# Kernel optimization log

Measured on AMD Instinct MI355X. Metric: run time of the kernel, lower is better.

## Reference

```python
import jax, jax.numpy as jnp
import numpy as np

PI = float(np.pi)


def _conv2d(x, w, b, pad):
    out = jax.lax.conv_general_dilated(x, w, (1, 1), ((pad, pad), (pad, pad)),
                                       dimension_numbers=('NCHW', 'OIHW', 'NCHW'))
    return out + b[None, :, None, None]


def _group_norm(x, gamma, beta, groups, eps=1e-5):
    B, C, h, w = x.shape
    xg = x.reshape(B, groups, C // groups, h, w)
    mu = xg.mean(axis=(2, 3, 4), keepdims=True)
    var = xg.var(axis=(2, 3, 4), keepdims=True)
    xn = ((xg - mu) / jnp.sqrt(var + eps)).reshape(B, C, h, w)
    return xn * gamma[None, :, None, None] + beta[None, :, None, None]


def _l2n(x, eps=1e-12):
    return x / jnp.maximum(jnp.linalg.norm(x, axis=1, keepdims=True), eps)


def _dense_sift(x):
    # kornia DenseSIFTDescriptor defaults: 8 ang bins, 4x4 spatial bins,
    # spatial_bin_size=4, rootsift=True, clipval=0.2, stride=1, padding=1
    eps = 1e-10
    NA = 8
    # 'diff' spatial gradient with replicate padding, normalized (/2)
    xp = jnp.pad(x, ((0, 0), (0, 0), (1, 1), (1, 1)), mode='edge')
    gx = (xp[:, :, 1:-1, 2:] - xp[:, :, 1:-1, :-2]) * 0.5
    gy = (xp[:, :, 2:, 1:-1] - xp[:, :, :-2, 1:-1]) * 0.5
    mag = jnp.sqrt(gx * gx + gy * gy + eps)[:, 0]           # [B,H,W]
    ori = jnp.arctan2(gy, gx + eps)[:, 0] + 2.0 * PI
    o_big = NA * ori / (2.0 * PI)
    bo0f = jnp.floor(o_big)
    wo1_ = o_big - bo0f
    wo0 = (1.0 - wo1_) * mag
    wo1 = wo1_ * mag
    bo0 = bo0f.astype(jnp.int32) % NA
    bo1 = (bo0 + 1) % NA
    bins = jnp.arange(NA).reshape(1, NA, 1, 1)
    ang = ((bo0[:, None] == bins).astype(x.dtype) * wo0[:, None]
           + (bo1[:, None] == bins).astype(x.dtype) * wo1[:, None])  # [B,8,H,W]
    # SIFT pooling kernel ksize=4 (triangle weights), conv pad=2 -> H+1,W+1
    xc2 = np.array([0.5, 1.5, 1.5, 0.5], np.float32)
    pool1 = np.outer(xc2, xc2) / 4.0
    pk = jnp.asarray(np.tile(pool1[None, None], (NA, 1, 1, 1)))  # depthwise [8,1,4,4]
    pooled = jax.lax.conv_general_dilated(ang, pk, (1, 1), ((2, 2), (2, 2)),
                dimension_numbers=('NCHW', 'OIHW', 'NCHW'), feature_group_count=NA)
    # identity reshape conv: 128 = 8 ang * 4*4 spatial bins, pad=1 -> back to H,W
    rk = jnp.asarray(np.eye(128, dtype=np.float32).reshape(128, NA, 4, 4))
    out = jax.lax.conv_general_dilated(pooled, rk, (1, 1), ((1, 1), (1, 1)),
                dimension_numbers=('NCHW', 'OIHW', 'NCHW'))
    out = jnp.clip(_l2n(out), 0.0, 0.2)
    out = _l2n(out)
    l1 = jnp.maximum(jnp.sum(jnp.abs(out), axis=1, keepdims=True), 1e-12)
    return jnp.sqrt(out / l1 + eps)  # rootsift


def _joint_bilateral(x, guide, ksize=5, sigma_color=0.1, sigma_space=1.5):
    pad = ksize // 2
    ax = np.arange(ksize, dtype=np.float32) - ksize // 2
    g1 = np.exp(-ax ** 2 / (2.0 * sigma_space ** 2))
    g1 = g1 / g1.sum()
    sk = np.outer(g1, g1)  # normalized 5x5 gaussian space kernel
    xp = jnp.pad(x, ((0, 0), (0, 0), (pad, pad), (pad, pad)), mode='reflect')
    gp = jnp.pad(guide, ((0, 0), (0, 0), (pad, pad), (pad, pad)), mode='reflect')
    h, w = x.shape[2], x.shape[3]
    inv = -0.5 / (sigma_color ** 2)
    num = jnp.zeros_like(x)
    den = jnp.zeros((x.shape[0], 1, h, w), x.dtype)
    for dy in range(ksize):           # fixed 5x5 tap loop, accumulated in-place
        for dx in range(ksize):
            gs = gp[:, :, dy:dy + h, dx:dx + w]
            cd = jnp.sum(jnp.abs(gs - guide), axis=1, keepdims=True) ** 2  # l1 squared
            wgt = sk[dy, dx] * jnp.exp(inv * cd)
            num = num + wgt * xp[:, :, dy:dy + h, dx:dx + w]
            den = den + wgt
    return num / den


def _forward(x, gt, w1, b1, g1w, g1b, w2, b2, g2w, g2b, w3, b3, g3w, g3b,
             w4, b4, g4w, g4b, w5, b5):
    orig = x
    f = _dense_sift(x)
    f = jax.nn.relu(_group_norm(_conv2d(f, w1, b1, 2), g1w, g1b, 8))
    f = jax.nn.relu(_group_norm(_conv2d(f, w2, b2, 1), g2w, g2b, 8))
    f = jax.nn.relu(_group_norm(_conv2d(f, w3, b3, 1), g3w, g3b, 4))
    f = jax.nn.relu(_group_norm(_conv2d(f, w4, b4, 1), g4w, g4b, 4))
    f = _conv2d(f, w5, b5, 1)
    # rgb_to_yuv(gt)[:, 1:] as guidance
    r, g, b = gt[:, 0], gt[:, 1], gt[:, 2]
    u = -0.147 * r - 0.289 * g + 0.436 * b
    v = 0.615 * r - 0.515 * g - 0.100 * b
    guide = jnp.stack([u, v], axis=1)
    f = _joint_bilateral(f, guide)

    def _rescale(c, lo, hi):
        c = (c - c.min()) / (c.max() - c.min() + 1e-6)  # global min/max over B,H,W
        c = jnp.clip(c, 0.0, 1.0)
        return c * (hi - lo) + lo

    U = _rescale(f[:, 0], -0.436, 0.436)
    V = _rescale(f[:, 1], -0.615, 0.615)
    Y = orig[:, 0]
    R = Y + 1.14 * V
    G = Y - 0.396 * U - 0.581 * V
    B = Y + 2.029 * U
    return jnp.stack([R, G, B], axis=1)


def setup_inputs() -> dict:
    key = jax.random.key(0)
    ks = jax.random.split(key, 16)
    B = 4
    d = {
        'x': jax.random.uniform(ks[0], (B, 1, 270, 512), jnp.float32),
        'gt': jax.random.uniform(ks[1], (B, 3, 270, 512), jnp.float32),
        'w1': jax.random.normal(ks[2], (64, 128, 5, 5), jnp.float32) * 0.02,
        'b1': jnp.zeros((64,), jnp.float32),
        'g1w': jnp.ones((64,), jnp.float32), 'g1b': jnp.zeros((64,), jnp.float32),
        'w2': jax.random.normal(ks[3], (32, 64, 3, 3), jnp.float32) * 0.04,
        'b2': jnp.zeros((32,), jnp.float32),
        'g2w': jnp.ones((32,), jnp.float32), 'g2b': jnp.zeros((32,), jnp.float32),
        'w3': jax.random.normal(ks[4], (16, 32, 3, 3), jnp.float32) * 0.05,
        'b3': jnp.zeros((16,), jnp.float32),
        'g3w': jnp.ones((16,), jnp.float32), 'g3b': jnp.zeros((16,), jnp.float32),
        'w4': jax.random.normal(ks[5], (8, 16, 3, 3), jnp.float32) * 0.08,
        'b4': jnp.zeros((8,), jnp.float32),
        'g4w': jnp.ones((8,), jnp.float32), 'g4b': jnp.zeros((8,), jnp.float32),
        'w5': jax.random.normal(ks[6], (2, 8, 3, 3), jnp.float32) * 0.1,
        'b5': jnp.zeros((2,), jnp.float32),
    }
    return d


def reference(x, gt, w1, b1, g1w, g1b, w2, b2, g2w, g2b, w3, b3, g3w, g3b,
              w4, b4, g4w, g4b, w5, b5):
    return _forward(x, gt, w1, b1, g1w, g1b, w2, b2, g2w, g2b, w3, b3, g3w, g3b,
                    w4, b4, g4w, g4b, w5, b5)
```

## Files before the change

kernel.cpp:

```cpp
#include <hip/hip_runtime.h>

constexpr int NB  = 4;
constexpr int IH  = 270;
constexpr int IW  = 512;
constexpr int NPIX = IH * IW;
constexpr int PH  = 271;
constexpr int PW  = 513;
constexpr float TWO_PI_F = 6.28318530717958647692f;

typedef short  bf16x8 __attribute__((ext_vector_type(8)));
typedef float floatx4 __attribute__((ext_vector_type(4)));

__device__ inline short f2bf(float x) {
  union { float f; unsigned u; } un; un.f = x;
  unsigned r = un.u + 0x7fff + ((un.u >> 16) & 1);
  return (short)(r >> 16);
}

__global__ __launch_bounds__(256) void pooled_kernel(
    const float* __restrict__ x, float* __restrict__ pooled) {
  const int b = blockIdx.z;
  const int px0 = blockIdx.x * 16, py0 = blockIdx.y * 16;
  __shared__ float wo0s[19][19];
  __shared__ float wo1s[19][19];
  __shared__ int   bo0s[19][19];
  const float* xb = x + (size_t)b * NPIX;

  for (int t = threadIdx.x; t < 19 * 19; t += 256) {
    int r = t / 19, c = t % 19;
    int gy = py0 - 2 + r, gx = px0 - 2 + c;
    float w0 = 0.f, w1v = 0.f; int b0 = 0;
    if (gy >= 0 && gy < IH && gx >= 0 && gx < IW) {
      int xm = gx > 0 ? gx - 1 : 0, xp = gx < IW - 1 ? gx + 1 : IW - 1;
      int ym = gy > 0 ? gy - 1 : 0, yp = gy < IH - 1 ? gy + 1 : IH - 1;
      float gxv = (xb[gy * IW + xp] - xb[gy * IW + xm]) * 0.5f;
      float gyv = (xb[yp * IW + gx] - xb[ym * IW + gx]) * 0.5f;
      float mag = sqrtf(gxv * gxv + gyv * gyv + 1e-10f);
      float ori = atan2f(gyv, gxv + 1e-10f) + TWO_PI_F;
      float obig = ori * (8.0f / TWO_PI_F);
      float bf = floorf(obig);
      float w1_ = obig - bf;
      w0  = (1.0f - w1_) * mag;
      w1v = w1_ * mag;
      b0  = ((int)bf) & 7;
    }
    wo0s[r][c] = w0; wo1s[r][c] = w1v; bo0s[r][c] = b0;
  }
  __syncthreads();

  const int t = threadIdx.x;
  const int lx = t % 16, ly = t / 16;
  const int py = py0 + ly, px = px0 + lx;
  if (py >= PH || px >= PW) return;

  const float pwt[4] = {0.25f, 0.75f, 0.75f, 0.25f};
  float acc[8] = {0, 0, 0, 0, 0, 0, 0, 0};
  for (int i = 0; i < 4; i++) {
    for (int j = 0; j < 4; j++) {
      int r = ly + i, c = lx + j;
      float w0 = wo0s[r][c], w1v = wo1s[r][c];
      int b0 = bo0s[r][c];
      int b1i = (b0 + 1) & 7;
      float pw = pwt[i] * pwt[j];
      #pragma unroll
      for (int a = 0; a < 8; a++) {
        float add = (a == b0 ? w0 : 0.f) + (a == b1i ? w1v : 0.f);
        acc[a] = fmaf(pw, add, acc[a]);
      }
    }
  }
  float* pb = pooled + (size_t)b * 8 * PH * PW;
  #pragma unroll
  for (int a = 0; a < 8; a++) pb[((size_t)a * PH + py) * PW + px] = acc[a];
}

__global__ __launch_bounds__(256) void sift_scalars_kernel(
    const float* __restrict__ pooled, float* __restrict__ s1g) {
  const int b = blockIdx.z;
  const int x0 = blockIdx.x * 16, y0 = blockIdx.y * 16;
  __shared__ float pt[8][19][19];
  const float* pb = pooled + (size_t)b * 8 * PH * PW;
  for (int t = threadIdx.x; t < 8 * 19 * 19; t += 256) {
    int a = t / 361, rc = t % 361, r = rc / 19, c = rc % 19;
    int gy = y0 - 1 + r, gx = x0 - 1 + c;
    float v = 0.f;
    if (gy >= 0 && gy < PH && gx >= 0 && gx < PW) v = pb[((size_t)a * PH + gy) * PW + gx];
    pt[a][r][c] = v;
  }
  __syncthreads();
  const int t = threadIdx.x;
  const int lx = t % 16, ly = t / 16;
  const int y = y0 + ly, x = x0 + lx;
  if (y >= IH) return;

  float sum2 = 0.f;
  for (int c = 0; c < 128; c++) {
    int a = c >> 4, i = (c >> 2) & 3, j = c & 3;
    float p = pt[a][ly + i][lx + j];
    sum2 = fmaf(p, p, sum2);
  }
  float s1 = 1.0f / fmaxf(sqrtf(sum2), 1e-12f);
  float st2 = 0.f, st = 0.f;
  for (int c = 0; c < 128; c++) {
    int a = c >> 4, i = (c >> 2) & 3, j = c & 3;
    float p = pt[a][ly + i][lx + j];
    float tv = fminf(p * s1, 0.2f);
    st2 = fmaf(tv, tv, st2);
    st += tv;
  }
  float s2 = 1.0f / fmaxf(sqrtf(st2), 1e-12f);
  float l1 = fmaxf(s2 * st, 1e-12f);
  float g = s2 / l1;
  float* o = s1g + (size_t)b * 2 * NPIX;
  o[y * IW + x] = s1;
  o[NPIX + y * IW + x] = g;
}

__global__ void repack_kernel(const float* __restrict__ w, float* __restrict__ wT,
                              int CO, int CI, int KK) {
  int i = blockIdx.x * 256 + threadIdx.x;
  int total = CO * CI * KK;
  if (i >= total) return;
  int o = i / (CI * KK);
  int r = i % (CI * KK);
  int ci = r / KK, kk = r % KK;
  wT[(kk * CI + ci) * CO + o] = w[i];
}

__global__ void mfma_pack_kernel(const float* __restrict__ w, short* __restrict__ wB,
                                 int CO, int CI, int KK) {
  int CHUNKS = (CI + 31) / 32;
  int GG = (CO + 15) / 16;
  int total = GG * CHUNKS * KK * 512;
  for (int i = blockIdx.x * 256 + threadIdx.x; i < total; i += gridDim.x * 256) {
    int j = i & 7, l = (i >> 3) & 63, f = i >> 9;
    int t = f % KK; int fc = f / KK; int cc = fc % CHUNKS; int g = fc / CHUNKS;
    int ci = cc * 32 + ((l >> 4) << 3) + j;
    int co = g * 16 + (l & 15);
    float v = (ci < CI && co < CO) ? w[((size_t)co * CI + ci) * KK + t] : 0.f;
    wB[i] = f2bf(v);
  }
}

__global__ __launch_bounds__(256) void conv1_mfma_kernel(
    const float* __restrict__ pooled, const float* __restrict__ s1g,
    const short* __restrict__ w1B, const float* __restrict__ bias,
    float* __restrict__ out, float* __restrict__ stats) {
  const int b = blockIdx.z;
  const int x0 = blockIdx.x * 16, y0 = blockIdx.y * 16;
  __shared__ __align__(16) char smem_raw[52128];
  short* desc = (short*)smem_raw;
  float* pt   = (float*)(smem_raw + 32000);
  float* sc   = (float*)(smem_raw + 48928);
  float* cout = (float*)smem_raw;

  const int tid = threadIdx.x;
  const int wave = tid >> 6, lane = tid & 63;
  const int quad = lane >> 4, lm = lane & 15;
  const int mh = wave & 1, pp = wave >> 1;

  const float* pb = pooled + (size_t)b * 8 * PH * PW;
  for (int t = tid; t < 8 * 23 * 23; t += 256) {
    int a = t / 529, rc = t % 529, r = rc / 23, c = rc % 23;
    int gy = y0 - 3 + r, gx = x0 - 3 + c;
    float v = 0.f;
    if (gy >= 0 && gy < PH && gx >= 0 && gx < PW) v = pb[((size_t)a * PH + gy) * PW + gx];
    pt[t] = v;
  }
  const float* sb = s1g + (size_t)b * 2 * NPIX;
  for (int t = tid; t < 400; t += 256) {
    int r = t / 20, c = t % 20;
    int gy = y0 - 2 + r, gx = x0 - 2 + c;
    float a0 = 0.f, a1 = 0.f;
    if (gy >= 0 && gy < IH && gx >= 0 && gx < IW) {
      a0 = sb[gy * IW + gx];
      a1 = sb[NPIX + gy * IW + gx];
    }
    sc[t] = a0; sc[400 + t] = a1;
  }

  const int laneoff = lm * 40 + quad * 8;
  floatx4 acc[2][8];
  #pragma unroll
  for (int n = 0; n < 2; n++)
    #pragma unroll
    for (int m = 0; m < 8; m++) acc[n][m] = (floatx4){0.f, 0.f, 0.f, 0.f};

  for (int cc = 0; cc < 4; cc++) {
    __syncthreads();
    for (int v = tid; v < 3200; v += 256) {
      int pos = v % 400, cg = v / 400;
      int r = pos / 20, c = pos % 20;
      int gy = y0 - 2 + r, gx = x0 - 2 + c;
      bool ok = (gy >= 0 && gy < IH && gx >= 0 && gx < IW);
      int ci0 = cc * 32 + cg * 4;
      int a = ci0 >> 4, i = (ci0 >> 2) & 3;
      float s1v = sc[pos], gv = sc[400 + pos];
      const float* prow = pt + a * 529 + (r + i) * 23 + c;
      unsigned short o4[4];
      #pragma unroll
      for (int q = 0; q < 4; q++) {
        float p = prow[q];
        float val = ok ? sqrtf(fminf(p * s1v, 0.2f) * gv + 1e-10f) : 0.f;
        o4[q] = (unsigned short)f2bf(val);
      }
      uint2 pk;
      pk.x = (unsigned)o4[0] | ((unsigned)o4[1] << 16);
      pk.y = (unsigned)o4[2] | ((unsigned)o4[3] << 16);
      *(uint2*)(desc + pos * 40 + cg * 4) = pk;
    }
    __syncthreads();

    #pragma unroll
    for (int ky = 0; ky < 5; ky++) {
      #pragma unroll
      for (int kx = 0; kx < 5; kx++) {
        bf16x8 bfr[2];
        #pragma unroll
        for (int ng = 0; ng < 2; ng++) {
          int f = ((pp * 2 + ng) * 4 + cc) * 25 + ky * 5 + kx;
          bfr[ng] = *(const bf16x8*)(w1B + ((size_t)f << 9) + (lane << 3));
        }
        bf16x8 av[8];
        #pragma unroll
        for (int m = 0; m < 8; m++) {
          int mt = mh * 8 + m;
          av[m] = *(const bf16x8*)(desc + (mt + ky) * 800 + kx * 40 + laneoff);
        }
        #pragma unroll
        for (int ng = 0; ng < 2; ng++)
          #pragma unroll
          for (int m = 0; m < 8; m++)
            acc[ng][m] = __builtin_amdgcn_mfma_f32_16x16x32_bf16(av[m], bfr[ng], acc[ng][m], 0, 0, 0);
      }
    }
  }

  float* ob = out + (size_t)b * 64 * NPIX;
  for (int h = 0; h < 2; h++) {
    __syncthreads();
    if (pp == h) {
      #pragma unroll
      for (int ng = 0; ng < 2; ng++)
        #pragma unroll
        for (int m = 0; m < 8; m++)
          #pragma unroll
          for (int r = 0; r < 4; r++)
            cout[(ng * 16 + lm) * 261 + (mh * 8 + m) * 16 + quad * 4 + r] = acc[ng][m][r];
    }
    __syncthreads();
    for (int v = tid; v < 8192; v += 256) {
      int col = v >> 8, px = v & 255;
      int y = y0 + (px >> 4), x = x0 + (px & 15);
      if (y < IH)
        ob[(size_t)(h * 32 + col) * NPIX + y * IW + x] = cout[col * 261 + px] + bias[h * 32 + col];
    }
    int col = tid >> 3, seg = tid & 7;
    int co = h * 32 + col;
    float bv = bias[co];
    float sum = 0.f, sq = 0.f;
    #pragma unroll
    for (int rr = 0; rr < 2; rr++) {
      int row = seg * 2 + rr;
      if (y0 + row < IH) {
        #pragma unroll
        for (int k = 0; k < 16; k++) {
          float vv = cout[col * 261 + row * 16 + k] + bv;
          sum += vv; sq += vv * vv;
        }
      }
    }
    sum += __shfl_down(sum, 4); sq += __shfl_down(sq, 4);
    sum += __shfl_down(sum, 2); sq += __shfl_down(sq, 2);
    sum += __shfl_down(sum, 1); sq += __shfl_down(sq, 1);
    if ((tid & 7) == 0) {
      atomicAdd(&stats[(b * 64 + co) * 2], sum);
      atomicAdd(&stats[(b * 64 + co) * 2 + 1], sq);
    }
  }
}

template <int CI, int CO, bool STATS>
__global__ __launch_bounds__(256) void convk3_mfma_kernel(
    const float* __restrict__ xin, const short* __restrict__ wB,
    const float* __restrict__ bias, const float* __restrict__ cA,
    const float* __restrict__ cB, float* __restrict__ stats,
    float* __restrict__ out) {
  constexpr int CHUNKS = CI / 32;
  constexpr int G = CO / 16;
  constexpr int WPG = 4 / G;
  constexpr int TPW = G;
  constexpr int CIS = CHUNKS * 32 + 8;
  const int b = blockIdx.z;
  const int x0 = blockIdx.x * 8, y0 = blockIdx.y * 8;
  __shared__ __align__(16) short tile[100 * CIS];
  __shared__ float cout[CO * 65];
  const int tid = threadIdx.x;
  const int wave = tid >> 6, lane = tid & 63;
  const int quad = lane >> 4, lm = lane & 15;
  const int g = wave / WPG, mh = wave % WPG;

  const float* xb = xin + (size_t)b * CI * NPIX;
  const float* cAb = cA + b * CI;
  const float* cBb = cB + b * CI;
  for (int v = tid; v < (CI / 2) * 100; v += 256) {
    int cp = v / 100, pos = v % 100;
    int r = pos / 10, c = pos % 10;
    int gy = y0 - 1 + r, gx = x0 - 1 + c;
    float v0 = 0.f, v1 = 0.f;
    if (gy >= 0 && gy < IH && gx >= 0 && gx < IW) {
      v0 = fmaxf(fmaf(xb[(size_t)(2 * cp) * NPIX + gy * IW + gx], cAb[2 * cp], cBb[2 * cp]), 0.f);
      v1 = fmaxf(fmaf(xb[(size_t)(2 * cp + 1) * NPIX + gy * IW + gx], cAb[2 * cp + 1], cBb[2 * cp + 1]), 0.f);
    }
    unsigned pk = (unsigned)(unsigned short)f2bf(v0) |
                  ((unsigned)(unsigned short)f2bf(v1) << 16);
    *(unsigned*)(tile + pos * CIS + 2 * cp) = pk;
  }
  __syncthreads();

  int abase[TPW];
  #pragma unroll
  for (int i = 0; i < TPW; i++) {
    int pixel = (mh * TPW + i) * 16 + lm;
    abase[i] = ((pixel >> 3) * 10 + (pixel & 7)) * CIS + quad * 8;
  }

  floatx4 acc[TPW];
  #pragma unroll
  for (int i = 0; i < TPW; i++) acc[i] = (floatx4){0.f, 0.f, 0.f, 0.f};

  #pragma unroll
  for (int cc = 0; cc < CHUNKS; cc++) {
    #pragma unroll
    for (int ky = 0; ky < 3; ky++) {
      bf16x8 bfr[3];
      #pragma unroll
      for (int kx = 0; kx < 3; kx++) {
        int f = (g * CHUNKS + cc) * 9 + ky * 3 + kx;
        bfr[kx] = *(const bf16x8*)(wB + ((size_t)f << 9) + (lane << 3));
      }
      #pragma unroll
      for (int kx = 0; kx < 3; kx++) {
        #pragma unroll
        for (int i = 0; i < TPW; i++) {
          bf16x8 av = *(const bf16x8*)(tile + abase[i] + cc * 32 + (ky * 10 + kx) * CIS);
          acc[i] = __builtin_amdgcn_mfma_f32_16x16x32_bf16(av, bfr[kx], acc[i], 0, 0, 0);
        }
      }
    }
  }
  #pragma unroll
  for (int i = 0; i < TPW; i++) {
    #pragma unroll
    for (int r = 0; r < 4; r++) {
      int pixel = (mh * TPW + i) * 16 + quad * 4 + r;
      cout[(g * 16 + lm) * 65 + pixel] = acc[i][r];
    }
  }
  __syncthreads();
  float* ob = out + (size_t)b * CO * NPIX;
  for (int v = tid; v < CO * 64; v += 256) {
    int co = v >> 6, pix = v & 63;
    int y = y0 + (pix >> 3), x = x0 + (pix & 7);
    if (y < IH) ob[(size_t)co * NPIX + y * IW + x] = cout[co * 65 + pix] + bias[co];
  }
  if (STATS) {
    constexpr int TPC = 256 / CO;
    constexpr int PXT = 64 / TPC;
    int col = tid / TPC, seg = tid % TPC;
    float bv = bias[col];
    float sum = 0.f, sq = 0.f;
    for (int k = 0; k < PXT; k++) {
      int p = seg * PXT + k;
      if (y0 + (p >> 3) < IH) {
        float vv = cout[col * 65 + p] + bv;
        sum += vv; sq += vv * vv;
      }
    }
    #pragma unroll
    for (int off = TPC / 2; off > 0; off >>= 1) {
      sum += __shfl_down(sum, off);
      sq  += __shfl_down(sq, off);
    }
    if (seg == 0) {
      atomicAdd(&stats[(b * CO + col) * 2], sum);
      atomicAdd(&stats[(b * CO + col) * 2 + 1], sq);
    }
  }
}

template <int CI, int CO, int OPT, bool STATS>
__global__ __launch_bounds__(256) void convs_kernel(
    const float* __restrict__ xin, const float* __restrict__ wT,
    const float* __restrict__ bias, const float* __restrict__ cA,
    const float* __restrict__ cB, float* __restrict__ stats,
    float* __restrict__ out) {
  const int b = blockIdx.z;
  const int x0 = blockIdx.x * 8, y0 = blockIdx.y * 8;
  __shared__ float tile[CI][10][10];
  __shared__ float ssum[CO], ssq[CO];
  if (STATS && threadIdx.x < CO) { ssum[threadIdx.x] = 0.f; ssq[threadIdx.x] = 0.f; }
  const float* xb = xin + (size_t)b * CI * NPIX;
  const float* cAb = cA + b * CI;
  const float* cBb = cB + b * CI;
  for (int t = threadIdx.x; t < CI * 100; t += 256) {
    int ci = t / 100, rc = t % 100, r = rc / 10, c = rc % 10;
    int gy = y0 - 1 + r, gx = x0 - 1 + c;
    float v = 0.f;
    if (gy >= 0 && gy < IH && gx >= 0 && gx < IW)
      v = fmaxf(fmaf(xb[(size_t)ci * NPIX + gy * IW + gx], cAb[ci], cBb[ci]), 0.f);
    tile[ci][r][c] = v;
  }
  __syncthreads();
  const int t = threadIdx.x;
  const int px = t % 64, og = t / 64;
  const int pyy = px / 8, pxx = px % 8;
  const int oc0 = og * OPT;
  const int y = y0 + pyy, x = x0 + pxx;
  if (og < CO / OPT) {
    float acc[OPT] = {};
    for (int ky = 0; ky < 3; ky++) {
      for (int kx = 0; kx < 3; kx++) {
        const float* wrow = wT + (size_t)((ky * 3 + kx) * CI) * CO + oc0;
        for (int ci = 0; ci < CI; ci++) {
          float v = tile[ci][pyy + ky][pxx + kx];
          #pragma unroll
          for (int o = 0; o < OPT; o++) acc[o] = fmaf(v, wrow[ci * CO + o], acc[o]);
        }
      }
    }
    if (y < IH) {
      float* ob = out + (size_t)b * CO * NPIX;
      #pragma unroll
      for (int o = 0; o < OPT; o++) {
        float vv = acc[o] + bias[oc0 + o];
        ob[(size_t)(oc0 + o) * NPIX + y * IW + x] = vv;
        if (STATS) {
          atomicAdd(&ssum[oc0 + o], vv);
          atomicAdd(&ssq[oc0 + o], vv * vv);
        }
      }
    }
  }
  if (STATS) {
    __syncthreads();
    if (threadIdx.x < CO) {
      atomicAdd(&stats[(b * CO + threadIdx.x) * 2], ssum[threadIdx.x]);
      atomicAdd(&stats[(b * CO + threadIdx.x) * 2 + 1], ssq[threadIdx.x]);
    }
  }
}

__global__ void gn_coef_kernel(const float* __restrict__ stats,
                               const float* __restrict__ gamma,
                               const float* __restrict__ beta,
                               float* __restrict__ cA, float* __restrict__ cB,
                               int C, int chper) {
  int i = blockIdx.x * 64 + threadIdx.x;
  if (i >= NB * C) return;
  int b = i / C, c = i % C;
  int g0 = (c / chper) * chper;
  double S = 0.0, S2 = 0.0;
  for (int k = 0; k < chper; k++) {
    S  += (double)stats[(b * C + g0 + k) * 2];
    S2 += (double)stats[(b * C + g0 + k) * 2 + 1];
  }
  double Nd = (double)chper * NPIX;
  double mu = S / Nd;
  double var = S2 / Nd - mu * mu;
  double rstd = 1.0 / sqrt(var + 1e-5);
  float A = (float)rstd * gamma[c];
  cA[i] = A;
  cB[i] = beta[c] - (float)mu * A;
}

__global__ __launch_bounds__(256) void bilateral_kernel(
    const float* __restrict__ f, const float* __restrict__ gt,
    float* __restrict__ out) {
  const int b = blockIdx.z;
  const int x0 = blockIdx.x * 16, y0 = blockIdx.y * 16;
  __shared__ float gu[20][20], gv[20][20], f0s[20][20], f1s[20][20];
  const float* gtb = gt + (size_t)b * 3 * NPIX;
  const float* fb = f + (size_t)b * 2 * NPIX;
  for (int t = threadIdx.x; t < 400; t += 256) {
    int r = t / 20, c = t % 20;
    int gy = y0 - 2 + r, gx = x0 - 2 + c;
    if (gy < 0) gy = -gy;
    if (gy > IH - 1) gy = 2 * (IH - 1) - gy;
    if (gx < 0) gx = -gx;
    if (gx > IW - 1) gx = 2 * (IW - 1) - gx;
    int p = gy * IW + gx;
    float rr = gtb[p], gg = gtb[NPIX + p], bb = gtb[2 * NPIX + p];
    gu[r][c]  = -0.147f * rr - 0.289f * gg + 0.436f * bb;
    gv[r][c]  =  0.615f * rr - 0.515f * gg - 0.100f * bb;
    f0s[r][c] = fb[p];
    f1s[r][c] = fb[NPIX + p];
  }
  __syncthreads();
  const int t = threadIdx.x;
  const int lx = t % 16, ly = t / 16;
  const int y = y0 + ly, x = x0 + lx;
  if (y >= IH) return;

  float g1v[5];
  {
    float s = 0.f;
    #pragma unroll
    for (int k = 0; k < 5; k++) {
      float a = (float)(k - 2);
      g1v[k] = expf(-a * a / 4.5f);
      s += g1v[k];
    }
    #pragma unroll
    for (int k = 0; k < 5; k++) g1v[k] /= s;
  }
  float cu = gu[ly + 2][lx + 2], cv = gv[ly + 2][lx + 2];
  float num0 = 0.f, num1 = 0.f, den = 0.f;
  #pragma unroll
  for (int dy = 0; dy < 5; dy++) {
    #pragma unroll
    for (int dx = 0; dx < 5; dx++) {
      float du = fabsf(gu[ly + dy][lx + dx] - cu) + fabsf(gv[ly + dy][lx + dx] - cv);
      float wgt = g1v[dy] * g1v[dx] * expf(-50.0f * du * du);
      num0 = fmaf(wgt, f0s[ly + dy][lx + dx], num0);
      num1 = fmaf(wgt, f1s[ly + dy][lx + dx], num1);
      den += wgt;
    }
  }
  float* ob = out + (size_t)b * 2 * NPIX;
  ob[y * IW + x] = num0 / den;
  ob[NPIX + y * IW + x] = num1 / den;
}

__global__ __launch_bounds__(256) void minmax_partial_kernel(
    const float* __restrict__ bil, float* __restrict__ part) {
  float mn0 = 1e30f, mx0 = -1e30f, mn1 = 1e30f, mx1 = -1e30f;
  for (size_t i = (size_t)blockIdx.x * 256 + threadIdx.x; i < (size_t)NB * NPIX;
       i += 256 * 256) {
    int b = (int)(i / NPIX), p = (int)(i % NPIX);
    float v0 = bil[(size_t)b * 2 * NPIX + p];
    float v1 = bil[(size_t)b * 2 * NPIX + NPIX + p];
    mn0 = fminf(mn0, v0); mx0 = fmaxf(mx0, v0);
    mn1 = fminf(mn1, v1); mx1 = fmaxf(mx1, v1);
  }
  __shared__ float sh[4][256];
  sh[0][threadIdx.x] = mn0; sh[1][threadIdx.x] = mx0;
  sh[2][threadIdx.x] = mn1; sh[3][threadIdx.x] = mx1;
  __syncthreads();
  for (int off = 128; off > 0; off >>= 1) {
    if (threadIdx.x < off) {
      sh[0][threadIdx.x] = fminf(sh[0][threadIdx.x], sh[0][threadIdx.x + off]);
      sh[1][threadIdx.x] = fmaxf(sh[1][threadIdx.x], sh[1][threadIdx.x + off]);
      sh[2][threadIdx.x] = fminf(sh[2][threadIdx.x], sh[2][threadIdx.x + off]);
      sh[3][threadIdx.x] = fmaxf(sh[3][threadIdx.x], sh[3][threadIdx.x + off]);
    }
    __syncthreads();
  }
  if (threadIdx.x == 0) {
    part[blockIdx.x * 4 + 0] = sh[0][0];
    part[blockIdx.x * 4 + 1] = sh[1][0];
    part[blockIdx.x * 4 + 2] = sh[2][0];
    part[blockIdx.x * 4 + 3] = sh[3][0];
  }
}

__global__ __launch_bounds__(256) void minmax_final_kernel(
    const float* __restrict__ part, float* __restrict__ mm) {
  __shared__ float sh[4][256];
  int t = threadIdx.x;
  sh[0][t] = part[t * 4 + 0];
  sh[1][t] = part[t * 4 + 1];
  sh[2][t] = part[t * 4 + 2];
  sh[3][t] = part[t * 4 + 3];
  __syncthreads();
  for (int off = 128; off > 0; off >>= 1) {
    if (t < off) {
      sh[0][t] = fminf(sh[0][t], sh[0][t + off]);
      sh[1][t] = fmaxf(sh[1][t], sh[1][t + off]);
      sh[2][t] = fminf(sh[2][t], sh[2][t + off]);
      sh[3][t] = fmaxf(sh[3][t], sh[3][t + off]);
    }
    __syncthreads();
  }
  if (t == 0) {
    mm[0] = sh[0][0]; mm[1] = sh[1][0]; mm[2] = sh[2][0]; mm[3] = sh[3][0];
  }
}

__global__ __launch_bounds__(256) void final_kernel(
    const float* __restrict__ bil, const float* __restrict__ x,
    const float* __restrict__ mm, float* __restrict__ out) {
  int i = blockIdx.x * 256 + threadIdx.x;
  if (i >= NB * NPIX) return;
  int b = i / NPIX, p = i % NPIX;
  float f0 = bil[(size_t)b * 2 * NPIX + p];
  float f1 = bil[(size_t)b * 2 * NPIX + NPIX + p];
  float U = (f0 - mm[0]) / (mm[1] - mm[0] + 1e-6f);
  U = fminf(fmaxf(U, 0.f), 1.f) * 0.872f - 0.436f;
  float V = (f1 - mm[2]) / (mm[3] - mm[2] + 1e-6f);
  V = fminf(fmaxf(V, 0.f), 1.f) * 1.23f - 0.615f;
  float Y = x[(size_t)b * NPIX + p];
  float* ob = out + (size_t)b * 3 * NPIX;
  ob[p]            = Y + 1.14f * V;
  ob[NPIX + p]     = Y - 0.396f * U - 0.581f * V;
  ob[2 * NPIX + p] = Y + 2.029f * U;
}

extern "C" void kernel_launch(void* const* d_in, const int* in_sizes, int n_in,
                              void* d_out, int out_size, void* d_ws, size_t ws_size,
                              hipStream_t stream) {
  const float* x   = (const float*)d_in[0];
  const float* gt  = (const float*)d_in[1];
  const float* w1  = (const float*)d_in[2];
  const float* b1  = (const float*)d_in[3];
  const float* g1w = (const float*)d_in[4];
  const float* g1b = (const float*)d_in[5];
  const float* w2  = (const float*)d_in[6];
  const float* b2  = (const float*)d_in[7];
  const float* g2w = (const float*)d_in[8];
  const float* g2b = (const float*)d_in[9];
  const float* w3  = (const float*)d_in[10];
  const float* b3  = (const float*)d_in[11];
  const float* g3w = (const float*)d_in[12];
  const float* g3b = (const float*)d_in[13];
  const float* w4  = (const float*)d_in[14];
  const float* b4  = (const float*)d_in[15];
  const float* g4w = (const float*)d_in[16];
  const float* g4b = (const float*)d_in[17];
  const float* w5  = (const float*)d_in[18];
  const float* b5  = (const float*)d_in[19];
  float* out = (float*)d_out;

  char* ws = (char*)d_ws;
  float* statsF = (float*)ws;
  float* stats1 = statsF;
  float* stats2 = statsF + 512;
  float* stats3 = statsF + 768;
  float* stats4 = statsF + 896;
  float* c1A = (float*)(ws + 4096);
  float* c1B = c1A + 256;
  float* c2A = c1B + 256;
  float* c2B = c2A + 128;
  float* c3A = c2B + 128;
  float* c3B = c3A + 64;
  float* c4A = c3B + 64;
  float* c4B = c4A + 32;
  float* mmpart = (float*)(ws + 8192);
  float* mm     = (float*)(ws + 12288);
  float* fbase  = (float*)(ws + 16384);
  size_t off = 0;
  float* pooled = fbase + off; off += 4452864;
  float* s1g    = fbase + off; off += 1105920;
  short* w1B    = (short*)(fbase + off); off += 102400;
  short* w2B    = (short*)(fbase + off); off += 9216;
  short* w3B    = (short*)(fbase + off); off += 2304;
  float* w4T    = fbase + off; off += 1152;
  float* w5T    = fbase + off; off += 256;
  float* bufA   = fbase + off; off += 35389440;
  float* bufB   = fbase + off; off += 17694720;
  float* c5     = pooled;
  float* bilat  = pooled + 1105920;

  hipMemsetAsync(statsF, 0, 960 * sizeof(float), stream);

  mfma_pack_kernel<<<800, 256, 0, stream>>>(w1, w1B, 64, 128, 25);
  mfma_pack_kernel<<<72, 256, 0, stream>>>(w2, w2B, 32, 64, 9);
  mfma_pack_kernel<<<18, 256, 0, stream>>>(w3, w3B, 16, 32, 9);
  repack_kernel<<<(8 * 16 * 9 + 255) / 256, 256, 0, stream>>>(w4, w4T, 8, 16, 9);
  repack_kernel<<<(2 * 8 * 9 + 255) / 256, 256, 0, stream>>>(w5, w5T, 2, 8, 9);

  pooled_kernel<<<dim3(33, 17, NB), 256, 0, stream>>>(x, pooled);
  sift_scalars_kernel<<<dim3(32, 17, NB), 256, 0, stream>>>(pooled, s1g);
  conv1_mfma_kernel<<<dim3(32, 17, NB), 256, 0, stream>>>(pooled, s1g, w1B, b1, bufA, stats1);
  gn_coef_kernel<<<(NB * 64 + 63) / 64, 64, 0, stream>>>(stats1, g1w, g1b, c1A, c1B, 64, 8);

  convk3_mfma_kernel<64, 32, true><<<dim3(64, 34, NB), 256, 0, stream>>>(
      bufA, w2B, b2, c1A, c1B, stats2, bufB);
  gn_coef_kernel<<<(NB * 32 + 63) / 64, 64, 0, stream>>>(stats2, g2w, g2b, c2A, c2B, 32, 4);

  convk3_mfma_kernel<32, 16, true><<<dim3(64, 34, NB), 256, 0, stream>>>(
      bufB, w3B, b3, c2A, c2B, stats3, bufA);
  gn_coef_kernel<<<(NB * 16 + 63) / 64, 64, 0, stream>>>(stats3, g3w, g3b, c3A, c3B, 16, 4);

  convs_kernel<16, 8, 2, true><<<dim3(64, 34, NB), 256, 0, stream>>>(
      bufA, w4T, b4, c3A, c3B, stats4, bufB);
  gn_coef_kernel<<<(NB * 8 + 63) / 64, 64, 0, stream>>>(stats4, g4w, g4b, c4A, c4B, 8, 2);

  convs_kernel<8, 2, 1, false><<<dim3(64, 34, NB), 256, 0, stream>>>(
      bufB, w5T, b5, c4A, c4B, nullptr, c5);

  bilateral_kernel<<<dim3(32, 17, NB), 256, 0, stream>>>(c5, gt, bilat);
  minmax_partial_kernel<<<256, 256, 0, stream>>>(bilat, mmpart);
  minmax_final_kernel<<<1, 256, 0, stream>>>(mmpart, mm);
  final_kernel<<<(NB * NPIX + 255) / 256, 256, 0, stream>>>(bilat, x, mm, out);

  (void)in_sizes; (void)n_in; (void)out_size; (void)ws_size;
}
```

Baseline: 1.555 ms.

## Fuse GN coefficients, weight packing and min/max into neighbouring kernels; retile convs

Merges the five weight-repack launches into one prep kernel and computes the GroupNorm coefficients inside each consumer conv kernel, which removes the separate gn_coef launches. The min/max reduction now happens in the bilateral kernel through wave shuffles and ordered-key atomics, replacing two reduction kernels. Conv1 stages pooled planes per channel chunk to cut shared memory, adds an occupancy hint and re-splits the MFMA tiles across waves. The 3x3 convs move to 16x8 output tiles to get more reuse per block. The cost is redundant coefficient math in every block, extra atomics, and a different register/LDS balance.

```diff
diff --git a/kernel.cpp b/kernel.cpp
--- a/kernel.cpp
+++ b/kernel.cpp
@@ -15,6 +15,74 @@
   union { float f; unsigned u; } un; un.f = x;
   unsigned r = un.u + 0x7fff + ((un.u >> 16) & 1);
   return (short)(r >> 16);
+}
+__device__ inline unsigned fkey(float f) {
+  unsigned u = __float_as_uint(f);
+  return (u & 0x80000000u) ? ~u : (u | 0x80000000u);
+}
+__device__ inline float funkey(unsigned k) {
+  unsigned u = (k & 0x80000000u) ? (k ^ 0x80000000u) : ~k;
+  return __uint_as_float(u);
+}
+__device__ inline void gn_coef_thread(const float* __restrict__ stats,
+                                      const float* __restrict__ gamma,
+                                      const float* __restrict__ beta,
+                                      float* cA, float* cB, int C, int chper, int b) {
+  int c = threadIdx.x;
+  if (c < C) {
+    int g0 = (c / chper) * chper;
+    float S = 0.f, S2 = 0.f;
+    for (int k = 0; k < chper; k++) {
+      S  += stats[(b * C + g0 + k) * 2];
+      S2 += stats[(b * C + g0 + k) * 2 + 1];
+    }
+    double Nd = (double)chper * NPIX;
+    double mu = (double)S / Nd;
+    double var = (double)S2 / Nd - mu * mu;
+    double rstd = 1.0 / sqrt(var + 1e-5);
+    float A = (float)rstd * gamma[c];
+    cA[c] = A;
+    cB[c] = beta[c] - (float)mu * A;
+  }
+}
+
+__device__ inline void mfma_pack_one(const float* __restrict__ w, short* __restrict__ wB,
+                                     int i, int CO, int CI, int KK, int CHUNKS) {
+  int j = i & 7, l = (i >> 3) & 63, f = i >> 9;
+  int t = f % KK; int fc = f / KK; int cc = fc % CHUNKS; int g = fc / CHUNKS;
+  int ci = cc * 32 + ((l >> 4) << 3) + j;
+  int co = g * 16 + (l & 15);
+  float v = (ci < CI && co < CO) ? w[((size_t)co * CI + ci) * KK + t] : 0.f;
+  wB[i] = f2bf(v);
+}
+__device__ inline void repack_one(const float* __restrict__ w, float* __restrict__ wT,
+                                  int i, int CO, int CI, int KK) {
+  int o = i / (CI * KK);
+  int r = i % (CI * KK);
+  int ci = r / KK, kk = r % KK;
+  wT[(kk * CI + ci) * CO + o] = w[i];
+}
+__global__ __launch_bounds__(256) void prep_kernel(
+    const float* __restrict__ w1, const float* __restrict__ w2,
+    const float* __restrict__ w3, const float* __restrict__ w4,
+    const float* __restrict__ w5,
+    short* __restrict__ w1B, short* __restrict__ w2B, short* __restrict__ w3B,
+    float* __restrict__ w4T, float* __restrict__ w5T) {
+  constexpr int N1 = 4 * 4 * 25 * 512;
+  constexpr int N2 = 2 * 2 * 9 * 512;
+  constexpr int N3 = 1 * 1 * 9 * 512;
+  constexpr int N4 = 8 * 16 * 9;
+  constexpr int N5 = 2 * 8 * 9;
+  int i = blockIdx.x * 256 + threadIdx.x;
+  if (i < N1) { mfma_pack_one(w1, w1B, i, 64, 128, 25, 4); return; }
+  i -= N1;
+  if (i < N2) { mfma_pack_one(w2, w2B, i, 32, 64, 9, 2); return; }
+  i -= N2;
+  if (i < N3) { mfma_pack_one(w3, w3B, i, 16, 32, 9, 1); return; }
+  i -= N3;
+  if (i < N4) { repack_one(w4, w4T, i, 8, 16, 9); return; }
+  i -= N4;
+  if (i < N5) { repack_one(w5, w5T, i, 2, 8, 9); return; }
 }
 
 __global__ __launch_bounds__(256) void pooled_kernel(
@@ -116,57 +184,23 @@
   o[NPIX + y * IW + x] = g;
 }
 
-__global__ void repack_kernel(const float* __restrict__ w, float* __restrict__ wT,
-                              int CO, int CI, int KK) {
-  int i = blockIdx.x * 256 + threadIdx.x;
-  int total = CO * CI * KK;
-  if (i >= total) return;
-  int o = i / (CI * KK);
-  int r = i % (CI * KK);
-  int ci = r / KK, kk = r % KK;
-  wT[(kk * CI + ci) * CO + o] = w[i];
-}
-
-__global__ void mfma_pack_kernel(const float* __restrict__ w, short* __restrict__ wB,
-                                 int CO, int CI, int KK) {
-  int CHUNKS = (CI + 31) / 32;
-  int GG = (CO + 15) / 16;
-  int total = GG * CHUNKS * KK * 512;
-  for (int i = blockIdx.x * 256 + threadIdx.x; i < total; i += gridDim.x * 256) {
-    int j = i & 7, l = (i >> 3) & 63, f = i >> 9;
-    int t = f % KK; int fc = f / KK; int cc = fc % CHUNKS; int g = fc / CHUNKS;
-    int ci = cc * 32 + ((l >> 4) << 3) + j;
-    int co = g * 16 + (l & 15);
-    float v = (ci < CI && co < CO) ? w[((size_t)co * CI + ci) * KK + t] : 0.f;
-    wB[i] = f2bf(v);
-  }
-}
-
-__global__ __launch_bounds__(256) void conv1_mfma_kernel(
+__global__ __launch_bounds__(256, 4) void conv1_mfma_kernel(
     const float* __restrict__ pooled, const float* __restrict__ s1g,
     const short* __restrict__ w1B, const float* __restrict__ bias,
     float* __restrict__ out, float* __restrict__ stats) {
   const int b = blockIdx.z;
   const int x0 = blockIdx.x * 16, y0 = blockIdx.y * 16;
-  __shared__ __align__(16) char smem_raw[52128];
+  __shared__ __align__(16) char smem_raw[39440];
   short* desc = (short*)smem_raw;
-  float* pt   = (float*)(smem_raw + 32000);
-  float* sc   = (float*)(smem_raw + 48928);
+  float* sc   = (float*)(smem_raw + 32000);
+  float* pt   = (float*)(smem_raw + 35208);
   float* cout = (float*)smem_raw;
 
   const int tid = threadIdx.x;
   const int wave = tid >> 6, lane = tid & 63;
   const int quad = lane >> 4, lm = lane & 15;
-  const int mh = wave & 1, pp = wave >> 1;
 
   const float* pb = pooled + (size_t)b * 8 * PH * PW;
-  for (int t = tid; t < 8 * 23 * 23; t += 256) {
-    int a = t / 529, rc = t % 529, r = rc / 23, c = rc % 23;
-    int gy = y0 - 3 + r, gx = x0 - 3 + c;
-    float v = 0.f;
-    if (gy >= 0 && gy < PH && gx >= 0 && gx < PW) v = pb[((size_t)a * PH + gy) * PW + gx];
-    pt[t] = v;
-  }
   const float* sb = s1g + (size_t)b * 2 * NPIX;
   for (int t = tid; t < 400; t += 256) {
     int r = t / 20, c = t % 20;
@@ -178,13 +212,19 @@
     }
     sc[t] = a0; sc[400 + t] = a1;
   }
-
-  const int laneoff = lm * 40 + quad * 8;
-  floatx4 acc[2][8];
+  for (int t = tid; t < 1058; t += 256) {
+    int pl = t / 529, rc = t % 529, r = rc / 23, c = rc % 23;
+    int gy = y0 - 3 + r, gx = x0 - 3 + c;
+    float v = 0.f;
+    if (gy >= 0 && gy < PH && gx >= 0 && gx < PW) v = pb[((size_t)pl * PH + gy) * PW + gx];
+    pt[t] = v;
+  }
+
+  floatx4 acc[4][4];
   #pragma unroll
-  for (int n = 0; n < 2; n++)
-    #pragma unroll
-    for (int m = 0; m < 8; m++) acc[n][m] = (floatx4){0.f, 0.f, 0.f, 0.f};
+  for (int n = 0; n < 4; n++)
+    #pragma unroll
+    for (int i = 0; i < 4; i++) acc[n][i] = (floatx4){0.f, 0.f, 0.f, 0.f};
 
   for (int cc = 0; cc < 4; cc++) {
     __syncthreads();
@@ -193,10 +233,10 @@
       int r = pos / 20, c = pos % 20;
       int gy = y0 - 2 + r, gx = x0 - 2 + c;
       bool ok = (gy >= 0 && gy < IH && gx >= 0 && gx < IW);
-      int ci0 = cc * 32 + cg * 4;
-      int a = ci0 >> 4, i = (ci0 >> 2) & 3;
+      int al = cg >> 2;
+      int ii = cg & 3;
       float s1v = sc[pos], gv = sc[400 + pos];
-      const float* prow = pt + a * 529 + (r + i) * 23 + c;
+      const float* prow = pt + al * 529 + (r + ii) * 23 + c;
       unsigned short o4[4];
       #pragma unroll
       for (int q = 0; q < 4; q++) {
@@ -211,27 +251,38 @@
     }
     __syncthreads();
 
+    if (cc < 3) {
+      for (int t = tid; t < 1058; t += 256) {
+        int pl = t / 529, rc = t % 529, r = rc / 23, c = rc % 23;
+        int gy = y0 - 3 + r, gx = x0 - 3 + c;
+        float v = 0.f;
+        if (gy >= 0 && gy < PH && gx >= 0 && gx < PW)
+          v = pb[((size_t)(2 * (cc + 1) + pl) * PH + gy) * PW + gx];
+        pt[t] = v;
+      }
+    }
+
     #pragma unroll
     for (int ky = 0; ky < 5; ky++) {
       #pragma unroll
       for (int kx = 0; kx < 5; kx++) {
-        bf16x8 bfr[2];
+        bf16x8 bfr[4];
         #pragma unroll
-        for (int ng = 0; ng < 2; ng++) {
-          int f = ((pp * 2 + ng) * 4 + cc) * 25 + ky * 5 + kx;
-          bfr[ng] = *(const bf16x8*)(w1B + ((size_t)f << 9) + (lane << 3));
+        for (int n = 0; n < 4; n++) {
+          int f = (n * 4 + cc) * 25 + ky * 5 + kx;
+          bfr[n] = *(const bf16x8*)(w1B + ((size_t)f << 9) + (lane << 3));
         }
-        bf16x8 av[8];
+        bf16x8 av[4];
         #pragma unroll
-        for (int m = 0; m < 8; m++) {
-          int mt = mh * 8 + m;
-          av[m] = *(const bf16x8*)(desc + (mt + ky) * 800 + kx * 40 + laneoff);
+        for (int i = 0; i < 4; i++) {
+          int mt = wave * 4 + i;
+          av[i] = *(const bf16x8*)(desc + ((mt + ky) * 20 + lm + kx) * 40 + quad * 8);
         }
         #pragma unroll
-        for (int ng = 0; ng < 2; ng++)
+        for (int n = 0; n < 4; n++)
           #pragma unroll
-          for (int m = 0; m < 8; m++)
-            acc[ng][m] = __builtin_amdgcn_mfma_f32_16x16x32_bf16(av[m], bfr[ng], acc[ng][m], 0, 0, 0);
+          for (int i = 0; i < 4; i++)
+            acc[n][i] = __builtin_amdgcn_mfma_f32_16x16x32_bf16(av[i], bfr[n], acc[n][i], 0, 0, 0);
       }
     }
   }
@@ -239,15 +290,13 @@
   float* ob = out + (size_t)b * 64 * NPIX;
   for (int h = 0; h < 2; h++) {
     __syncthreads();
-    if (pp == h) {
+    #pragma unroll
+    for (int nn = 0; nn < 2; nn++)
       #pragma unroll
-      for (int ng = 0; ng < 2; ng++)
+      for (int i = 0; i < 4; i++)
         #pragma unroll
-        for (int m = 0; m < 8; m++)
-          #pragma unroll
-          for (int r = 0; r < 4; r++)
-            cout[(ng * 16 + lm) * 261 + (mh * 8 + m) * 16 + quad * 4 + r] = acc[ng][m][r];
-    }
+        for (int r = 0; r < 4; r++)
+          cout[(nn * 16 + lm) * 261 + (wave * 4 + i) * 16 + quad * 4 + r] = acc[h * 2 + nn][i][r];
     __syncthreads();
     for (int v = tid; v < 8192; v += 256) {
       int col = v >> 8, px = v & 255;
@@ -280,37 +329,44 @@
   }
 }
 
-template <int CI, int CO, bool STATS>
+template <int CI, int CO, int CHPER, bool STATS>
 __global__ __launch_bounds__(256) void convk3_mfma_kernel(
     const float* __restrict__ xin, const short* __restrict__ wB,
-    const float* __restrict__ bias, const float* __restrict__ cA,
-    const float* __restrict__ cB, float* __restrict__ stats,
-    float* __restrict__ out) {
+    const float* __restrict__ bias, const float* __restrict__ statsIn,
+    const float* __restrict__ gamma, const float* __restrict__ beta,
+    float* __restrict__ statsOut, float* __restrict__ out) {
   constexpr int CHUNKS = CI / 32;
   constexpr int G = CO / 16;
-  constexpr int WPG = 4 / G;
-  constexpr int TPW = G;
-  constexpr int CIS = CHUNKS * 32 + 8;
+  constexpr int MPW = 2 * G;
+  constexpr int CIS = CI + 8;
+  constexpr int TILE_B = 180 * CIS * 2;
+  constexpr int COUT_B = CO * 133 * 4;
+  constexpr int UNION_B = TILE_B > COUT_B ? TILE_B : COUT_B;
+  __shared__ __align__(16) char sm[UNION_B + CI * 8];
+  short* tile = (short*)sm;
+  float* cout = (float*)sm;
+  float* cA = (float*)(sm + UNION_B);
+  float* cB = cA + CI;
+
   const int b = blockIdx.z;
-  const int x0 = blockIdx.x * 8, y0 = blockIdx.y * 8;
-  __shared__ __align__(16) short tile[100 * CIS];
-  __shared__ float cout[CO * 65];
+  const int x0 = blockIdx.x * 16, y0 = blockIdx.y * 8;
   const int tid = threadIdx.x;
   const int wave = tid >> 6, lane = tid & 63;
   const int quad = lane >> 4, lm = lane & 15;
-  const int g = wave / WPG, mh = wave % WPG;
+  const int n = wave % G, mh = wave / G;
+
+  gn_coef_thread(statsIn, gamma, beta, cA, cB, CI, CHPER, b);
+  __syncthreads();
 
   const float* xb = xin + (size_t)b * CI * NPIX;
-  const float* cAb = cA + b * CI;
-  const float* cBb = cB + b * CI;
-  for (int v = tid; v < (CI / 2) * 100; v += 256) {
-    int cp = v / 100, pos = v % 100;
-    int r = pos / 10, c = pos % 10;
+  for (int v = tid; v < (CI / 2) * 180; v += 256) {
+    int cp = v / 180, pos = v % 180;
+    int r = pos / 18, c = pos % 18;
     int gy = y0 - 1 + r, gx = x0 - 1 + c;
     float v0 = 0.f, v1 = 0.f;
     if (gy >= 0 && gy < IH && gx >= 0 && gx < IW) {
-      v0 = fmaxf(fmaf(xb[(size_t)(2 * cp) * NPIX + gy * IW + gx], cAb[2 * cp], cBb[2 * cp]), 0.f);
-      v1 = fmaxf(fmaf(xb[(size_t)(2 * cp + 1) * NPIX + gy * IW + gx], cAb[2 * cp + 1], cBb[2 * cp + 1]), 0.f);
+      v0 = fmaxf(fmaf(xb[(size_t)(2 * cp) * NPIX + gy * IW + gx], cA[2 * cp], cB[2 * cp]), 0.f);
+      v1 = fmaxf(fmaf(xb[(size_t)(2 * cp + 1) * NPIX + gy * IW + gx], cA[2 * cp + 1], cB[2 * cp + 1]), 0.f);
     }
     unsigned pk = (unsigned)(unsigned short)f2bf(v0) |
                   ((unsigned)(unsigned short)f2bf(v1) << 16);
@@ -318,62 +374,54 @@
   }
   __syncthreads();
 
-  int abase[TPW];
+  floatx4 acc[MPW];
   #pragma unroll
-  for (int i = 0; i < TPW; i++) {
-    int pixel = (mh * TPW + i) * 16 + lm;
-    abase[i] = ((pixel >> 3) * 10 + (pixel & 7)) * CIS + quad * 8;
-  }
-
-  floatx4 acc[TPW];
-  #pragma unroll
-  for (int i = 0; i < TPW; i++) acc[i] = (floatx4){0.f, 0.f, 0.f, 0.f};
+  for (int i = 0; i < MPW; i++) acc[i] = (floatx4){0.f, 0.f, 0.f, 0.f};
 
   #pragma unroll
   for (int cc = 0; cc < CHUNKS; cc++) {
     #pragma unroll
     for (int ky = 0; ky < 3; ky++) {
-      bf16x8 bfr[3];
       #pragma unroll
       for (int kx = 0; kx < 3; kx++) {
-        int f = (g * CHUNKS + cc) * 9 + ky * 3 + kx;
-        bfr[kx] = *(const bf16x8*)(wB + ((size_t)f << 9) + (lane << 3));
-      }
-      #pragma unroll
-      for (int kx = 0; kx < 3; kx++) {
+        int f = (n * CHUNKS + cc) * 9 + ky * 3 + kx;
+        bf16x8 bfr = *(const bf16x8*)(wB + ((size_t)f << 9) + (lane << 3));
         #pragma unroll
-        for (int i = 0; i < TPW; i++) {
-          bf16x8 av = *(const bf16x8*)(tile + abase[i] + cc * 32 + (ky * 10 + kx) * CIS);
-          acc[i] = __builtin_amdgcn_mfma_f32_16x16x32_bf16(av, bfr[kx], acc[i], 0, 0, 0);
+        for (int i = 0; i < MPW; i++) {
+          int mt = mh * MPW + i;
+          bf16x8 av = *(const bf16x8*)(tile + ((mt + ky) * 18 + lm + kx) * CIS + cc * 32 + quad * 8);
+          acc[i] = __builtin_amdgcn_mfma_f32_16x16x32_bf16(av, bfr, acc[i], 0, 0, 0);
         }
       }
     }
   }
+  __syncthreads();
   #pragma unroll
-  for (int i = 0; i < TPW; i++) {
+  for (int i = 0; i < MPW; i++) {
     #pragma unroll
     for (int r = 0; r < 4; r++) {
-      int pixel = (mh * TPW + i) * 16 + quad * 4 + r;
-      cout[(g * 16 + lm) * 65 + pixel] = acc[i][r];
+      int pixel = (mh * MPW + i) * 16 + quad * 4 + r;
+      cout[(n * 16 + lm) * 133 + pixel] = acc[i][r];
     }
   }
   __syncthreads();
   float* ob = out + (size_t)b * CO * NPIX;
-  for (int v = tid; v < CO * 64; v += 256) {
-    int co = v >> 6, pix = v & 63;
-    int y = y0 + (pix >> 3), x = x0 + (pix & 7);
-    if (y < IH) ob[(size_t)co * NPIX + y * IW + x] = cout[co * 65 + pix] + bias[co];
+  for (int v = tid; v < CO * 128; v += 256) {
+    int co = v >> 7, px = v & 127;
+    int y = y0 + (px >> 4), x = x0 + (px & 15);
+    if (y < IH) ob[(size_t)co * NPIX + y * IW + x] = cout[co * 133 + px] + bias[co];
   }
   if (STATS) {
     constexpr int TPC = 256 / CO;
-    constexpr int PXT = 64 / TPC;
+    constexpr int PXT = 128 / TPC;
     int col = tid / TPC, seg = tid % TPC;
     float bv = bias[col];
     float sum = 0.f, sq = 0.f;
+    #pragma unroll
     for (int k = 0; k < PXT; k++) {
       int p = seg * PXT + k;
-      if (y0 + (p >> 3) < IH) {
-        float vv = cout[col * 65 + p] + bv;
+      if (y0 + (p >> 4) < IH) {
+        float vv = cout[col * 133 + p] + bv;
         sum += vv; sq += vv * vv;
       }
     }
@@ -383,103 +431,81 @@
       sq  += __shfl_down(sq, off);
     }
     if (seg == 0) {
-      atomicAdd(&stats[(b * CO + col) * 2], sum);
-      atomicAdd(&stats[(b * CO + col) * 2 + 1], sq);
-    }
-  }
-}
-
-template <int CI, int CO, int OPT, bool STATS>
+      atomicAdd(&statsOut[(b * CO + col) * 2], sum);
+      atomicAdd(&statsOut[(b * CO + col) * 2 + 1], sq);
+    }
+  }
+}
+
+template <int CI, int CO, int CHPER, bool STATS>
 __global__ __launch_bounds__(256) void convs_kernel(
     const float* __restrict__ xin, const float* __restrict__ wT,
-    const float* __restrict__ bias, const float* __restrict__ cA,
-    const float* __restrict__ cB, float* __restrict__ stats,
-    float* __restrict__ out) {
+    const float* __restrict__ bias, const float* __restrict__ statsIn,
+    const float* __restrict__ gamma, const float* __restrict__ beta,
+    float* __restrict__ statsOut, float* __restrict__ out) {
+  constexpr int OPT = CO / 2;
   const int b = blockIdx.z;
-  const int x0 = blockIdx.x * 8, y0 = blockIdx.y * 8;
-  __shared__ float tile[CI][10][10];
+  const int x0 = blockIdx.x * 16, y0 = blockIdx.y * 8;
+  __shared__ float tile[CI * 180];
+  __shared__ float cA[CI], cB[CI];
   __shared__ float ssum[CO], ssq[CO];
+  gn_coef_thread(statsIn, gamma, beta, cA, cB, CI, CHPER, b);
   if (STATS && threadIdx.x < CO) { ssum[threadIdx.x] = 0.f; ssq[threadIdx.x] = 0.f; }
+  __syncthreads();
   const float* xb = xin + (size_t)b * CI * NPIX;
-  const float* cAb = cA + b * CI;
-  const float* cBb = cB + b * CI;
-  for (int t = threadIdx.x; t < CI * 100; t += 256) {
-    int ci = t / 100, rc = t % 100, r = rc / 10, c = rc % 10;
+  for (int t = threadIdx.x; t < CI * 180; t += 256) {
+    int ci = t / 180, rc = t % 180, r = rc / 18, c = rc % 18;
     int gy = y0 - 1 + r, gx = x0 - 1 + c;
     float v = 0.f;
     if (gy >= 0 && gy < IH && gx >= 0 && gx < IW)
-      v = fmaxf(fmaf(xb[(size_t)ci * NPIX + gy * IW + gx], cAb[ci], cBb[ci]), 0.f);
-    tile[ci][r][c] = v;
+      v = fmaxf(fmaf(xb[(size_t)ci * NPIX + gy * IW + gx], cA[ci], cB[ci]), 0.f);
+    tile[t] = v;
   }
   __syncthreads();
   const int t = threadIdx.x;
-  const int px = t % 64, og = t / 64;
-  const int pyy = px / 8, pxx = px % 8;
+  const int px = t & 127, og = t >> 7;
+  const int pyy = px >> 4, pxx = px & 15;
   const int oc0 = og * OPT;
   const int y = y0 + pyy, x = x0 + pxx;
-  if (og < CO / OPT) {
-    float acc[OPT] = {};
-    for (int ky = 0; ky < 3; ky++) {
-      for (int kx = 0; kx < 3; kx++) {
-        const float* wrow = wT + (size_t)((ky * 3 + kx) * CI) * CO + oc0;
-        for (int ci = 0; ci < CI; ci++) {
-          float v = tile[ci][pyy + ky][pxx + kx];
-          #pragma unroll
-          for (int o = 0; o < OPT; o++) acc[o] = fmaf(v, wrow[ci * CO + o], acc[o]);
-        }
-      }
-    }
-    if (y < IH) {
-      float* ob = out + (size_t)b * CO * NPIX;
-      #pragma unroll
-      for (int o = 0; o < OPT; o++) {
-        float vv = acc[o] + bias[oc0 + o];
-        ob[(size_t)(oc0 + o) * NPIX + y * IW + x] = vv;
-        if (STATS) {
-          atomicAdd(&ssum[oc0 + o], vv);
-          atomicAdd(&ssq[oc0 + o], vv * vv);
-        }
+  float acc[OPT] = {};
+  for (int ky = 0; ky < 3; ky++) {
+    for (int kx = 0; kx < 3; kx++) {
+      const float* wrow = wT + (size_t)((ky * 3 + kx) * CI) * CO + oc0;
+      for (int ci = 0; ci < CI; ci++) {
+        float v = tile[ci * 180 + (pyy + ky) * 18 + pxx + kx];
+        #pragma unroll
+        for (int o = 0; o < OPT; o++) acc[o] = fmaf(v, wrow[ci * CO + o], acc[o]);
+      }
+    }
+  }
+  if (y < IH) {
+    float* ob = out + (size_t)b * CO * NPIX;
+    #pragma unroll
+    for (int o = 0; o < OPT; o++) {
+      float vv = acc[o] + bias[oc0 + o];
+      ob[(size_t)(oc0 + o) * NPIX + y * IW + x] = vv;
+      if (STATS) {
+        atomicAdd(&ssum[oc0 + o], vv);
+        atomicAdd(&ssq[oc0 + o], vv * vv);
       }
     }
   }
   if (STATS) {
     __syncthreads();
     if (threadIdx.x < CO) {
-      atomicAdd(&stats[(b * CO + threadIdx.x) * 2], ssum[threadIdx.x]);
-      atomicAdd(&stats[(b * CO + threadIdx.x) * 2 + 1], ssq[threadIdx.x]);
-    }
-  }
-}
-
-__global__ void gn_coef_kernel(const float* __restrict__ stats,
-                               const float* __restrict__ gamma,
-                               const float* __restrict__ beta,
-                               float* __restrict__ cA, float* __restrict__ cB,
-                               int C, int chper) {
-  int i = blockIdx.x * 64 + threadIdx.x;
-  if (i >= NB * C) return;
-  int b = i / C, c = i % C;
-  int g0 = (c / chper) * chper;
-  double S = 0.0, S2 = 0.0;
-  for (int k = 0; k < chper; k++) {
-    S  += (double)stats[(b * C + g0 + k) * 2];
-    S2 += (double)stats[(b * C + g0 + k) * 2 + 1];
-  }
-  double Nd = (double)chper * NPIX;
-  double mu = S / Nd;
-  double var = S2 / Nd - mu * mu;
-  double rstd = 1.0 / sqrt(var + 1e-5);
-  float A = (float)rstd * gamma[c];
-  cA[i] = A;
-  cB[i] = beta[c] - (float)mu * A;
+      atomicAdd(&statsOut[(b * CO + threadIdx.x) * 2], ssum[threadIdx.x]);
+      atomicAdd(&statsOut[(b * CO + threadIdx.x) * 2 + 1], ssq[threadIdx.x]);
+    }
+  }
 }
 
 __global__ __launch_bounds__(256) void bilateral_kernel(
     const float* __restrict__ f, const float* __restrict__ gt,
-    float* __restrict__ out) {
+    float* __restrict__ out, unsigned* __restrict__ mmbits) {
   const int b = blockIdx.z;
   const int x0 = blockIdx.x * 16, y0 = blockIdx.y * 16;
   __shared__ float gu[20][20], gv[20][20], f0s[20][20], f1s[20][20];
+  __shared__ float red[4][4];
   const float* gtb = gt + (size_t)b * 3 * NPIX;
   const float* fb = f + (size_t)b * 2 * NPIX;
   for (int t = threadIdx.x; t < 400; t += 256) {
@@ -500,10 +526,11 @@
   const int t = threadIdx.x;
   const int lx = t % 16, ly = t / 16;
   const int y = y0 + ly, x = x0 + lx;
-  if (y >= IH) return;
-
-  float g1v[5];
-  {
+  const bool valid = (y < IH);
+
+  float o0 = 0.f, o1 = 0.f;
+  if (valid) {
+    float g1v[5];
     float s = 0.f;
     #pragma unroll
     for (int k = 0; k < 5; k++) {
@@ -513,91 +540,65 @@
     }
     #pragma unroll
     for (int k = 0; k < 5; k++) g1v[k] /= s;
-  }
-  float cu = gu[ly + 2][lx + 2], cv = gv[ly + 2][lx + 2];
-  float num0 = 0.f, num1 = 0.f, den = 0.f;
+    float cu = gu[ly + 2][lx + 2], cv = gv[ly + 2][lx + 2];
+    float num0 = 0.f, num1 = 0.f, den = 0.f;
+    #pragma unroll
+    for (int dy = 0; dy < 5; dy++) {
+      #pragma unroll
+      for (int dx = 0; dx < 5; dx++) {
+        float du = fabsf(gu[ly + dy][lx + dx] - cu) + fabsf(gv[ly + dy][lx + dx] - cv);
+        float wgt = g1v[dy] * g1v[dx] * expf(-50.0f * du * du);
+        num0 = fmaf(wgt, f0s[ly + dy][lx + dx], num0);
+        num1 = fmaf(wgt, f1s[ly + dy][lx + dx], num1);
+        den += wgt;
+      }
+    }
+    o0 = num0 / den; o1 = num1 / den;
+    float* ob = out + (size_t)b * 2 * NPIX;
+    ob[y * IW + x] = o0;
+    ob[NPIX + y * IW + x] = o1;
+  }
+  float mn0 = valid ? o0 : 1e30f,  mx0 = valid ? o0 : -1e30f;
+  float mn1 = valid ? o1 : 1e30f,  mx1 = valid ? o1 : -1e30f;
   #pragma unroll
-  for (int dy = 0; dy < 5; dy++) {
-    #pragma unroll
-    for (int dx = 0; dx < 5; dx++) {
-      float du = fabsf(gu[ly + dy][lx + dx] - cu) + fabsf(gv[ly + dy][lx + dx] - cv);
-      float wgt = g1v[dy] * g1v[dx] * expf(-50.0f * du * du);
-      num0 = fmaf(wgt, f0s[ly + dy][lx + dx], num0);
-      num1 = fmaf(wgt, f1s[ly + dy][lx + dx], num1);
-      den += wgt;
-    }
-  }
-  float* ob = out + (size_t)b * 2 * NPIX;
-  ob[y * IW + x] = num0 / den;
-  ob[NPIX + y * IW + x] = num1 / den;
-}
-
-__global__ __launch_bounds__(256) void minmax_partial_kernel(
-    const float* __restrict__ bil, float* __restrict__ part) {
-  float mn0 = 1e30f, mx0 = -1e30f, mn1 = 1e30f, mx1 = -1e30f;
-  for (size_t i = (size_t)blockIdx.x * 256 + threadIdx.x; i < (size_t)NB * NPIX;
-       i += 256 * 256) {
-    int b = (int)(i / NPIX), p = (int)(i % NPIX);
-    float v0 = bil[(size_t)b * 2 * NPIX + p];
-    float v1 = bil[(size_t)b * 2 * NPIX + NPIX + p];
-    mn0 = fminf(mn0, v0); mx0 = fmaxf(mx0, v0);
-    mn1 = fminf(mn1, v1); mx1 = fmaxf(mx1, v1);
-  }
-  __shared__ float sh[4][256];
-  sh[0][threadIdx.x] = mn0; sh[1][threadIdx.x] = mx0;
-  sh[2][threadIdx.x] = mn1; sh[3][threadIdx.x] = mx1;
-  __syncthreads();
-  for (int off = 128; off > 0; off >>= 1) {
-    if (threadIdx.x < off) {
-      sh[0][threadIdx.x] = fminf(sh[0][threadIdx.x], sh[0][threadIdx.x + off]);
-      sh[1][threadIdx.x] = fmaxf(sh[1][threadIdx.x], sh[1][threadIdx.x + off]);
-      sh[2][threadIdx.x] = fminf(sh[2][threadIdx.x], sh[2][threadIdx.x + off]);
-      sh[3][threadIdx.x] = fmaxf(sh[3][threadIdx.x], sh[3][threadIdx.x + off]);
-    }
-    __syncthreads();
-  }
-  if (threadIdx.x == 0) {
-    part[blockIdx.x * 4 + 0] = sh[0][0];
-    part[blockIdx.x * 4 + 1] = sh[1][0];
-    part[blockIdx.x * 4 + 2] = sh[2][0];
-    part[blockIdx.x * 4 + 3] = sh[3][0];
-  }
-}
-
-__global__ __launch_bounds__(256) void minmax_final_kernel(
-    const float* __restrict__ part, float* __restrict__ mm) {
-  __shared__ float sh[4][256];
-  int t = threadIdx.x;
-  sh[0][t] = part[t * 4 + 0];
-  sh[1][t] = part[t * 4 + 1];
-  sh[2][t] = part[t * 4 + 2];
-  sh[3][t] = part[t * 4 + 3];
-  __syncthreads();
-  for (int off = 128; off > 0; off >>= 1) {
-    if (t < off) {
-      sh[0][t] = fminf(sh[0][t], sh[0][t + off]);
-      sh[1][t] = fmaxf(sh[1][t], sh[1][t + off]);
-      sh[2][t] = fminf(sh[2][t], sh[2][t + off]);
-      sh[3][t] = fmaxf(sh[3][t], sh[3][t + off]);
-    }
-    __syncthreads();
-  }
+  for (int off = 32; off > 0; off >>= 1) {
+    mn0 = fminf(mn0, __shfl_xor(mn0, off));
+    mx0 = fmaxf(mx0, __shfl_xor(mx0, off));
+    mn1 = fminf(mn1, __shfl_xor(mn1, off));
+    mx1 = fmaxf(mx1, __shfl_xor(mx1, off));
+  }
+  if ((t & 63) == 0) {
+    red[t >> 6][0] = mn0; red[t >> 6][1] = mx0;
+    red[t >> 6][2] = mn1; red[t >> 6][3] = mx1;
+  }
+  __syncthreads();
   if (t == 0) {
-    mm[0] = sh[0][0]; mm[1] = sh[1][0]; mm[2] = sh[2][0]; mm[3] = sh[3][0];
+    for (int w = 1; w < 4; w++) {
+      red[0][0] = fminf(red[0][0], red[w][0]);
+      red[0][1] = fmaxf(red[0][1], red[w][1]);
+      red[0][2] = fminf(red[0][2], red[w][2]);
+      red[0][3] = fmaxf(red[0][3], red[w][3]);
+    }
+    atomicMax(&mmbits[0], fkey(red[0][1]));
+    atomicMax(&mmbits[1], fkey(red[0][3]));
+    atomicMin(&mmbits[2], fkey(red[0][0]));
+    atomicMin(&mmbits[3], fkey(red[0][2]));
   }
 }
 
 __global__ __launch_bounds__(256) void final_kernel(
     const float* __restrict__ bil, const float* __restrict__ x,
-    const float* __restrict__ mm, float* __restrict__ out) {
+    const unsigned* __restrict__ mmbits, float* __restrict__ out) {
   int i = blockIdx.x * 256 + threadIdx.x;
   if (i >= NB * NPIX) return;
+  float mx0 = funkey(mmbits[0]), mx1 = funkey(mmbits[1]);
+  float mn0 = funkey(mmbits[2]), mn1 = funkey(mmbits[3]);
   int b = i / NPIX, p = i % NPIX;
   float f0 = bil[(size_t)b * 2 * NPIX + p];
   float f1 = bil[(size_t)b * 2 * NPIX + NPIX + p];
-  float U = (f0 - mm[0]) / (mm[1] - mm[0] + 1e-6f);
+  float U = (f0 - mn0) / (mx0 - mn0 + 1e-6f);
   U = fminf(fmaxf(U, 0.f), 1.f) * 0.872f - 0.436f;
-  float V = (f1 - mm[2]) / (mm[3] - mm[2] + 1e-6f);
+  float V = (f1 - mn1) / (mx1 - mn1 + 1e-6f);
   V = fminf(fmaxf(V, 0.f), 1.f) * 1.23f - 0.615f;
   float Y = x[(size_t)b * NPIX + p];
   float* ob = out + (size_t)b * 3 * NPIX;
@@ -632,21 +633,11 @@
   float* out = (float*)d_out;
 
   char* ws = (char*)d_ws;
-  float* statsF = (float*)ws;
-  float* stats1 = statsF;
-  float* stats2 = statsF + 512;
-  float* stats3 = statsF + 768;
-  float* stats4 = statsF + 896;
-  float* c1A = (float*)(ws + 4096);
-  float* c1B = c1A + 256;
-  float* c2A = c1B + 256;
-  float* c2B = c2A + 128;
-  float* c3A = c2B + 128;
-  float* c3B = c3A + 64;
-  float* c4A = c3B + 64;
-  float* c4B = c4A + 32;
-  float* mmpart = (float*)(ws + 8192);
-  float* mm     = (float*)(ws + 12288);
+  float* stats1 = (float*)ws;
+  float* stats2 = stats1 + 512;
+  float* stats3 = stats2 + 256;
+  float* stats4 = stats3 + 128;
+  unsigned* mmbits = (unsigned*)(ws + 12288);
   float* fbase  = (float*)(ws + 16384);
   size_t off = 0;
   float* pooled = fbase + off; off += 4452864;
@@ -661,38 +652,29 @@
   float* c5     = pooled;
   float* bilat  = pooled + 1105920;
 
-  hipMemsetAsync(statsF, 0, 960 * sizeof(float), stream);
-
-  mfma_pack_kernel<<<800, 256, 0, stream>>>(w1, w1B, 64, 128, 25);
-  mfma_pack_kernel<<<72, 256, 0, stream>>>(w2, w2B, 32, 64, 9);
-  mfma_pack_kernel<<<18, 256, 0, stream>>>(w3, w3B, 16, 32, 9);
-  repack_kernel<<<(8 * 16 * 9 + 255) / 256, 256, 0, stream>>>(w4, w4T, 8, 16, 9);
-  repack_kernel<<<(2 * 8 * 9 + 255) / 256, 256, 0, stream>>>(w5, w5T, 2, 8, 9);
+  hipMemsetAsync(ws, 0, 12304, stream);
+  hipMemsetAsync(ws + 12296, 0xFF, 8, stream);
+
+  prep_kernel<<<896, 256, 0, stream>>>(w1, w2, w3, w4, w5, w1B, w2B, w3B, w4T, w5T);
 
   pooled_kernel<<<dim3(33, 17, NB), 256, 0, stream>>>(x, pooled);
   sift_scalars_kernel<<<dim3(32, 17, NB), 256, 0, stream>>>(pooled, s1g);
   conv1_mfma_kernel<<<dim3(32, 17, NB), 256, 0, stream>>>(pooled, s1g, w1B, b1, bufA, stats1);
-  gn_coef_kernel<<<(NB * 64 + 63) / 64, 64, 0, stream>>>(stats1, g1w, g1b, c1A, c1B, 64, 8);
-
-  convk3_mfma_kernel<64, 32, true><<<dim3(64, 34, NB), 256, 0, stream>>>(
-      bufA, w2B, b2, c1A, c1B, stats2, bufB);
-  gn_coef_kernel<<<(NB * 32 + 63) / 64, 64, 0, stream>>>(stats2, g2w, g2b, c2A, c2B, 32, 4);
-
-  convk3_mfma_kernel<32, 16, true><<<dim3(64, 34, NB), 256, 0, stream>>>(
-      bufB, w3B, b3, c2A, c2B, stats3, bufA);
-  gn_coef_kernel<<<(NB * 16 + 63) / 64, 64, 0, stream>>>(stats3, g3w, g3b, c3A, c3B, 16, 4);
-
-  convs_kernel<16, 8, 2, true><<<dim3(64, 34, NB), 256, 0, stream>>>(
-      bufA, w4T, b4, c3A, c3B, stats4, bufB);
-  gn_coef_kernel<<<(NB * 8 + 63) / 64, 64, 0, stream>>>(stats4, g4w, g4b, c4A, c4B, 8, 2);
-
-  convs_kernel<8, 2, 1, false><<<dim3(64, 34, NB), 256, 0, stream>>>(
-      bufB, w5T, b5, c4A, c4B, nullptr, c5);
-
-  bilateral_kernel<<<dim3(32, 17, NB), 256, 0, stream>>>(c5, gt, bilat);
-  minmax_partial_kernel<<<256, 256, 0, stream>>>(bilat, mmpart);
-  minmax_final_kernel<<<1, 256, 0, stream>>>(mmpart, mm);
-  final_kernel<<<(NB * NPIX + 255) / 256, 256, 0, stream>>>(bilat, x, mm, out);
+
+  convk3_mfma_kernel<64, 32, 8, true><<<dim3(32, 34, NB), 256, 0, stream>>>(
+      bufA, w2B, b2, stats1, g1w, g1b, stats2, bufB);
+
+  convk3_mfma_kernel<32, 16, 4, true><<<dim3(32, 34, NB), 256, 0, stream>>>(
+      bufB, w3B, b3, stats2, g2w, g2b, stats3, bufA);
+
+  convs_kernel<16, 8, 4, true><<<dim3(32, 34, NB), 256, 0, stream>>>(
+      bufA, w4T, b4, stats3, g3w, g3b, stats4, bufB);
+
+  convs_kernel<8, 2, 2, false><<<dim3(32, 34, NB), 256, 0, stream>>>(
+      bufB, w5T, b5, stats4, g4w, g4b, nullptr, c5);
+
+  bilateral_kernel<<<dim3(32, 17, NB), 256, 0, stream>>>(c5, gt, bilat, mmbits);
+  final_kernel<<<(NB * NPIX + 255) / 256, 256, 0, stream>>>(bilat, x, mmbits, out);
 
   (void)in_sizes; (void)n_in; (void)out_size; (void)ws_size;
 }
```

Measured after the change: 1.526 ms. About the same (-1.8%).
